# Kernel optimization log

Measured on AMD Instinct MI355X. Metric: run time of the kernel, lower is better.

Reference implementation:

```python
import jax, jax.numpy as jnp
import numpy as np

N, E, F_IN, NUM_GRAPHS, K = 50000, 500000, 160, 128, 3


def _glorot(k, shape):
    lim = np.sqrt(6.0 / (shape[-2] + shape[-1])).astype(np.float32)
    return jax.random.uniform(k, shape, jnp.float32, -lim, lim)


def setup_inputs() -> dict:
    key = jax.random.key(0)
    ks = jax.random.split(key, 8)
    x = jax.random.normal(ks[0], (N, F_IN), jnp.float32)
    edge_index = jax.random.randint(ks[1], (2, E), 0, N)
    edge_attr = jax.random.uniform(ks[2], (E,), jnp.float32)
    batch = jnp.sort(jax.random.randint(ks[3], (N,), 0, NUM_GRAPHS))
    W1 = _glorot(ks[4], (K, F_IN, 128)); b1 = jnp.zeros((128,), jnp.float32)
    W2 = _glorot(ks[5], (K, 128, 64)); b2 = jnp.zeros((64,), jnp.float32)
    W3 = _glorot(ks[6], (K, 64, 32)); b3 = jnp.zeros((32,), jnp.float32)
    Wl = _glorot(ks[7], (32, 2)); bl = jnp.zeros((2,), jnp.float32)
    return dict(x=x, edge_index=edge_index, edge_attr=edge_attr, batch=batch,
                W1=W1, b1=b1, W2=W2, b2=b2, W3=W3, b3=b3, Wl=Wl, bl=bl)


def _cheb_norm(src, dst, edge_attr, n):
    # PyG ChebConv: sym-normalized Laplacian, lambda_max=2 =>
    # L_hat = (2/lmax)*L_sym - I = -D^{-1/2} A D^{-1/2} (diagonal = 0)
    deg = jax.ops.segment_sum(edge_attr, src, num_segments=n)
    safe = jnp.where(deg > 0, deg, 1.0)
    dinv = jnp.where(deg > 0, jax.lax.rsqrt(safe), 0.0)
    return -dinv[src] * edge_attr * dinv[dst]


def _propagate(x, src, dst, w, n):
    # out[dst] += w * x[src]  (sparse L_hat @ x)
    return jax.ops.segment_sum(w[:, None] * x[src], dst, num_segments=n)


def _cheb_conv(x, src, dst, w, W, b, n):
    # Chebyshev recurrence: T0 = x, T1 = L_hat x, Tk = 2 L_hat T(k-1) - T(k-2)
    tx0 = x
    out = tx0 @ W[0]
    tx1 = _propagate(tx0, src, dst, w, n)
    out = out + tx1 @ W[1]
    for k in range(2, W.shape[0]):
        tx2 = 2.0 * _propagate(tx1, src, dst, w, n) - tx0
        out = out + tx2 @ W[k]
        tx0, tx1 = tx1, tx2
    return out + b


def reference(x, edge_index, edge_attr, batch, W1, b1, W2, b2, W3, b3, Wl, bl):
    n = x.shape[0]
    src, dst = edge_index[0], edge_index[1]
    w = _cheb_norm(src, dst, edge_attr, n)
    h = jax.nn.relu(_cheb_conv(x, src, dst, w, W1, b1, n))
    h = jax.nn.relu(_cheb_conv(h, src, dst, w, W2, b2, n))
    h = jax.nn.relu(_cheb_conv(h, src, dst, w, W3, b3, n))
    # global_mean_pool over graph ids (dropout omitted: eval mode)
    sums = jax.ops.segment_sum(h, batch, num_segments=NUM_GRAPHS)
    cnt = jax.ops.segment_sum(jnp.ones((n,), h.dtype), batch, num_segments=NUM_GRAPHS)
    pooled = sums / jnp.maximum(cnt, 1.0)[:, None]
    return pooled @ Wl + bl
```

## Files before the change

kernel.cpp:

```cpp
#include <hip/hip_runtime.h>

#define N_NODES 50000
#define N_EDGES 500000
#define NUM_G   128
#define SCAN_NB 49
#define PN      (SCAN_NB * 1024)
#define NCX     32
#define NCX_SH  5
#define ECH     15628
#define RNG     8192
#define NRY     7
#define HVB     (2 * NCX * NRY)
#define CONVB   7813
#define WPREPB  360
#define RNG_SC  2688
#define NRY_SC  19
#define SCVB    (NCX * NRY_SC)
#define GEMM_MB 782

typedef __attribute__((ext_vector_type(8))) short short8;
typedef __attribute__((ext_vector_type(4))) float f32x4;
typedef __attribute__((ext_vector_type(2))) float f32x2;

__device__ __forceinline__ unsigned f2bf(float x) {
    unsigned u = __float_as_uint(x);
    return (u + 0x7FFFu + ((u >> 16) & 1u)) >> 16;
}
__device__ __forceinline__ float bf2f(unsigned h) {
    return __uint_as_float(h << 16);
}

__device__ __forceinline__ void wprep_one(const float* __restrict__ W, unsigned short* __restrict__ WT,
                                          int t, int FIN, int F) {
    int n = t / FIN, k = t - n * FIN;
    int sel = n / F, c = n - sel * F;
    float v;
    if (sel == 0) v = W[(size_t)k * F + c] - W[(size_t)2 * FIN * F + (size_t)k * F + c];
    else          v = W[(size_t)sel * FIN * F + (size_t)k * F + c];
    WT[t] = (unsigned short)f2bf(v);
}

__global__ __launch_bounds__(256)
void prep_kernel(const int* __restrict__ src, const int* __restrict__ dst,
                 const float* __restrict__ ea,
                 float* __restrict__ pdeg, int* __restrict__ pcnt,
                 const float* __restrict__ x, unsigned short* __restrict__ Xb,
                 const float* __restrict__ W1, const float* __restrict__ W2,
                 const float* __restrict__ W3,
                 unsigned short* __restrict__ WT1, unsigned short* __restrict__ WT2,
                 unsigned short* __restrict__ WT3) {
    __shared__ unsigned lh[RNG];
    int vb = blockIdx.x, tid = threadIdx.x;
    if (vb < HVB) {
        bool isdeg = vb < NCX * NRY;
        int v2 = isdeg ? vb : vb - NCX * NRY;
        int xk = v2 & (NCX - 1), y = v2 >> NCX_SH;
        int base = y * RNG;
        for (int i = tid; i < RNG; i += 256) lh[i] = 0u;
        __syncthreads();
        int e0 = xk * ECH, e1 = min(e0 + ECH, N_EDGES);
        if (isdeg) {
            for (int e = e0 + tid * 4; e < e1; e += 1024) {
                int4 s4 = *reinterpret_cast<const int4*>(src + e);
                if ((unsigned)(s4.x - base) < RNG) atomicAdd((float*)&lh[s4.x - base], ea[e]);
                if ((unsigned)(s4.y - base) < RNG) atomicAdd((float*)&lh[s4.y - base], ea[e + 1]);
                if ((unsigned)(s4.z - base) < RNG) atomicAdd((float*)&lh[s4.z - base], ea[e + 2]);
                if ((unsigned)(s4.w - base) < RNG) atomicAdd((float*)&lh[s4.w - base], ea[e + 3]);
            }
        } else {
            for (int e = e0 + tid * 4; e < e1; e += 1024) {
                int4 d4 = *reinterpret_cast<const int4*>(dst + e);
                if ((unsigned)(d4.x - base) < RNG) atomicAdd((int*)&lh[d4.x - base], 1);
                if ((unsigned)(d4.y - base) < RNG) atomicAdd((int*)&lh[d4.y - base], 1);
                if ((unsigned)(d4.z - base) < RNG) atomicAdd((int*)&lh[d4.z - base], 1);
                if ((unsigned)(d4.w - base) < RNG) atomicAdd((int*)&lh[d4.w - base], 1);
            }
        }
        __syncthreads();
        if (isdeg) {
            for (int i = tid; i < RNG; i += 256) {
                int n = base + i;
                if (n < PN) pdeg[(size_t)xk * PN + n] = ((float*)lh)[i];
            }
        } else {
            for (int i = tid; i < RNG; i += 256) {
                int n = base + i;
                if (n < PN) pcnt[(size_t)xk * PN + n] = ((int*)lh)[i];
            }
        }
    } else if (vb < HVB + CONVB) {
        int t = (vb - HVB) * 256 + tid;
        if (t < N_NODES * 160 / 4) {
            float4 v = reinterpret_cast<const float4*>(x)[t];
            ushort4 r;
            r.x = (unsigned short)f2bf(v.x);
            r.y = (unsigned short)f2bf(v.y);
            r.z = (unsigned short)f2bf(v.z);
            r.w = (unsigned short)f2bf(v.w);
            *reinterpret_cast<ushort4*>(Xb + (size_t)t * 4) = r;
        }
    } else {
        int t = (vb - HVB - CONVB) * 256 + tid;
        if (t < 61440)      wprep_one(W1, WT1, t, 160, 128);
        else if (t < 86016) wprep_one(W2, WT2, t - 61440, 128, 64);
        else if (t < 92160) wprep_one(W3, WT3, t - 86016, 64, 32);
    }
}

__global__ __launch_bounds__(256)
void reduce_scan_kernel(const float* __restrict__ pdeg, int* __restrict__ pcnt,
                        float* __restrict__ dinv, int* __restrict__ cnt,
                        int* __restrict__ partial) {
    int b = blockIdx.x, t = threadIdx.x;
    int i0 = b * 1024 + t * 4;
    float d0 = 0.f, d1 = 0.f, d2 = 0.f, d3 = 0.f;
    int r0 = 0, r1 = 0, r2 = 0, r3 = 0;
    for (int x = 0; x < NCX; ++x) {
        float4 pv = *reinterpret_cast<const float4*>(pdeg + (size_t)x * PN + i0);
        int4   cv = *reinterpret_cast<const int4*>(pcnt + (size_t)x * PN + i0);
        *reinterpret_cast<int4*>(pcnt + (size_t)x * PN + i0) = make_int4(r0, r1, r2, r3);
        d0 += pv.x; d1 += pv.y; d2 += pv.z; d3 += pv.w;
        r0 += cv.x; r1 += cv.y; r2 += cv.z; r3 += cv.w;
    }
    float dd[4] = {d0, d1, d2, d3};
    int   rr[4] = {r0, r1, r2, r3};
    int s = 0;
    #pragma unroll
    for (int j = 0; j < 4; ++j) {
        int n = i0 + j;
        if (n < N_NODES) {
            float dv = dd[j], r = 0.f;
            if (dv > 0.f) {
                r = rsqrtf(dv);
                r = r * (1.5f - 0.5f * dv * r * r);
            }
            dinv[n] = r;
            cnt[n] = rr[j];
            s += rr[j];
        } else {
            cnt[n] = 0;
        }
    }
    __shared__ int red[256];
    red[t] = s;
    __syncthreads();
    for (int off = 128; off > 0; off >>= 1) {
        if (t < off) red[t] += red[t + off];
        __syncthreads();
    }
    if (t == 0) partial[b] = red[0];
}

__global__ __launch_bounds__(256)
void scan_final_kernel(const int* __restrict__ cnt, const int* __restrict__ partial,
                       int* __restrict__ rowptr, int n) {
    int b = blockIdx.x, t = threadIdx.x;
    __shared__ int red[256];
    __shared__ int sh_off, sh_tot;
    if (t < 64) {
        int orig = (t < SCAN_NB) ? partial[t] : 0;
        int v = orig;
        #pragma unroll
        for (int off = 1; off < 64; off <<= 1) {
            int u = __shfl_up(v, off, 64);
            if (t >= off) v += u;
        }
        if (t == b) sh_off = v - orig;
        if (t == SCAN_NB - 1) sh_tot = v;
    }
    __syncthreads();
    int4 v = reinterpret_cast<const int4*>(cnt)[b * 256 + t];
    int s = v.x + v.y + v.z + v.w;
    red[t] = s;
    __syncthreads();
    for (int off = 1; off < 256; off <<= 1) {
        int u = (t >= off) ? red[t - off] : 0;
        __syncthreads();
        red[t] += u;
        __syncthreads();
    }
    int excl = sh_off + ((t == 0) ? 0 : red[t - 1]);
    int i0 = b * 1024 + t * 4;
    if (i0 < n)     rowptr[i0]     = excl;
    if (i0 + 1 < n) rowptr[i0 + 1] = excl + v.x;
    if (i0 + 2 < n) rowptr[i0 + 2] = excl + v.x + v.y;
    if (i0 + 3 < n) rowptr[i0 + 3] = excl + v.x + v.y + v.z;
    if (b == SCAN_NB - 1 && t == 0) rowptr[n] = sh_tot;
}

__device__ void scatter_body(int vb, const int* __restrict__ src, const int* __restrict__ dst,
                             const float* __restrict__ ea,
                             const int* __restrict__ rowptr, const int* __restrict__ pcnt,
                             int2* __restrict__ csr, unsigned char* smraw) {
    int* cursor = (int*)smraw;
    int tid = threadIdx.x;
    int x = vb & (NCX - 1), y = vb >> NCX_SH;
    int base = y * RNG_SC;
    for (int i = tid; i < RNG_SC; i += 256) {
        int n = base + i;
        cursor[i] = (n < N_NODES) ? (rowptr[n] + pcnt[(size_t)x * PN + n]) : 0;
    }
    __syncthreads();
    int e0 = x * ECH, e1 = min(e0 + ECH, N_EDGES);
    for (int e = e0 + tid * 4; e < e1; e += 1024) {
        int4 d4 = *reinterpret_cast<const int4*>(dst + e);
        if ((unsigned)(d4.x - base) < RNG_SC) {
            int pos = atomicAdd(&cursor[d4.x - base], 1);
            csr[pos] = make_int2(src[e], __float_as_int(ea[e]));
        }
        if ((unsigned)(d4.y - base) < RNG_SC) {
            int pos = atomicAdd(&cursor[d4.y - base], 1);
            csr[pos] = make_int2(src[e + 1], __float_as_int(ea[e + 1]));
        }
        if ((unsigned)(d4.z - base) < RNG_SC) {
            int pos = atomicAdd(&cursor[d4.z - base], 1);
            csr[pos] = make_int2(src[e + 2], __float_as_int(ea[e + 2]));
        }
        if ((unsigned)(d4.w - base) < RNG_SC) {
            int pos = atomicAdd(&cursor[d4.w - base], 1);
            csr[pos] = make_int2(src[e + 3], __float_as_int(ea[e + 3]));
        }
    }
}

template<int FIN, int F>
__device__ void gemm_body(int bx, const unsigned short* __restrict__ Xb,
                          const unsigned short* __restrict__ WT, const float* __restrict__ dinv,
                          unsigned short* __restrict__ Y0, unsigned short* __restrict__ Y1,
                          unsigned short* __restrict__ Y2, int nrows, unsigned char* smraw) {
    constexpr int KT = FIN / 32;
    constexpr int NT = F / 32;
    constexpr int NTT = 3 * NT;
    constexpr int SA = FIN + 8;
    constexpr int F8 = FIN / 8;
    short* Bs = (short*)smraw;

    int tid = threadIdx.x;
    int lane = tid & 63, w = tid >> 6;
    int m0 = bx * 64;

    int colb = lane & 15;
    int q8 = (lane >> 4) << 3;
    int rq = (lane >> 4) << 2;
    int arow = m0 + w * 16 + colb;
    bool rok = arow < nrows;

    short8 afr[KT];
    #pragma unroll
    for (int kt = 0; kt < KT; ++kt) {
        short8 z = {0, 0, 0, 0, 0, 0, 0, 0};
        afr[kt] = rok ? *reinterpret_cast<const short8*>(Xb + (size_t)arow * FIN + (kt << 5) + q8) : z;
    }

    for (int nt = 0; nt < NTT; ++nt) {
        int n0 = nt << 5;
        __syncthreads();
        for (int span = tid; span < 32 * F8; span += 256) {
            int r = span / F8, c8 = (span - r * F8) << 3;
            int pr = (r < 16) ? (r << 1) : (((r - 16) << 1) + 1);
            *reinterpret_cast<uint4*>(&Bs[r * SA + c8]) =
                *reinterpret_cast<const uint4*>(WT + (size_t)(n0 + pr) * FIN + c8);
        }
        __syncthreads();

        f32x4 acc0 = {0.f, 0.f, 0.f, 0.f}, acc1 = acc0;
        #pragma unroll
        for (int kt = 0; kt < KT; ++kt) {
            short8 b0 = *reinterpret_cast<const short8*>(&Bs[colb * SA + (kt << 5) + q8]);
            short8 b1 = *reinterpret_cast<const short8*>(&Bs[(colb + 16) * SA + (kt << 5) + q8]);
            acc0 = __builtin_amdgcn_mfma_f32_16x16x32_bf16(afr[kt], b0, acc0, 0, 0, 0);
            acc1 = __builtin_amdgcn_mfma_f32_16x16x32_bf16(afr[kt], b1, acc1, 0, 0, 0);
        }

        int g = nt / NT;
        int ntg = nt - g * NT;
        unsigned short* Ys = (g == 0) ? Y0 : (g == 1) ? Y1 : Y2;
        int lc = (ntg << 5) + (colb << 1);
        #pragma unroll
        for (int r = 0; r < 4; ++r) {
            int orow = m0 + w * 16 + rq + r;
            if (orow < nrows) {
                float sc = (g == 2) ? dinv[orow] : 1.0f;
                unsigned pack = f2bf(acc0[r] * sc) | (f2bf(acc1[r] * sc) << 16);
                *reinterpret_cast<unsigned*>(Ys + (size_t)orow * F + lc) = pack;
            }
        }
    }
}

__global__ __launch_bounds__(256)
void sg_kernel(const int* __restrict__ src, const int* __restrict__ dst,
               const float* __restrict__ ea,
               const int* __restrict__ rowptr, const int* __restrict__ pcnt,
               int2* __restrict__ csr,
               const unsigned short* __restrict__ Xb, const unsigned short* __restrict__ WT1,
               const float* __restrict__ dinv,
               unsigned short* __restrict__ Y0, unsigned short* __restrict__ Y1,
               unsigned short* __restrict__ Y2) {
    __shared__ alignas(16) unsigned char sm[32 * (160 + 8) * 2];
    int vb = blockIdx.x;
    if (vb < SCVB) {
        scatter_body(vb, src, dst, ea, rowptr, pcnt, csr, sm);
    } else {
        gemm_body<160, 128>(vb - SCVB, Xb, WT1, dinv, Y0, Y1, Y2, N_NODES, sm);
    }
}

template<int FIN, int F>
__launch_bounds__(256)
__global__ void cheb_gemm(const unsigned short* __restrict__ Xb, const unsigned short* __restrict__ WT,
                          const float* __restrict__ dinv,
                          unsigned short* __restrict__ Y0, unsigned short* __restrict__ Y1,
                          unsigned short* __restrict__ Y2, int nrows) {
    __shared__ alignas(16) unsigned char sm[32 * (FIN + 8) * 2];
    gemm_body<FIN, F>(blockIdx.x, Xb, WT, dinv, Y0, Y1, Y2, nrows, sm);
}

__device__ __forceinline__ void acc8p(f32x2* acc, uint4 p, float wv) {
    f32x2 w2; w2[0] = wv; w2[1] = wv;
    f32x2 a0, a1, a2, a3;
    a0[0] = __uint_as_float(p.x << 16); a0[1] = __uint_as_float(p.x & 0xFFFF0000u);
    a1[0] = __uint_as_float(p.y << 16); a1[1] = __uint_as_float(p.y & 0xFFFF0000u);
    a2[0] = __uint_as_float(p.z << 16); a2[1] = __uint_as_float(p.z & 0xFFFF0000u);
    a3[0] = __uint_as_float(p.w << 16); a3[1] = __uint_as_float(p.w & 0xFFFF0000u);
    acc[0] += w2 * a0;
    acc[1] += w2 * a1;
    acc[2] += w2 * a2;
    acc[3] += w2 * a3;
}

__device__ __forceinline__ void expand8(uint4 p, float* o) {
    o[0] = bf2f(p.x & 0xFFFFu);
    o[1] = __uint_as_float(p.x & 0xFFFF0000u);
    o[2] = bf2f(p.y & 0xFFFFu);
    o[3] = __uint_as_float(p.y & 0xFFFF0000u);
    o[4] = bf2f(p.z & 0xFFFFu);
    o[5] = __uint_as_float(p.z & 0xFFFF0000u);
    o[6] = bf2f(p.w & 0xFFFFu);
    o[7] = __uint_as_float(p.w & 0xFFFF0000u);
}

template<int F, int MODE>
__launch_bounds__(256)
__global__ void gather_kernel(const unsigned short* __restrict__ X, const int2* __restrict__ csr,
                              const int* __restrict__ rowptr, const float* __restrict__ dinv,
                              const unsigned short* __restrict__ Y, const float* __restrict__ bias,
                              unsigned short* __restrict__ O, int n) {
    constexpr int FQ8 = F >> 3;
    constexpr int DPB = 256 / FQ8;
    constexpr int CAP = 1280;
    __shared__ int2 scsr[CAP];
    __shared__ int srp[DPB + 1];
    __shared__ int smap[DPB];
    int tid = threadIdx.x;
    int db0 = blockIdx.x * DPB;
    if (tid <= DPB) srp[tid] = rowptr[min(db0 + tid, n)];
    __syncthreads();
    int ebeg = srp[0];
    int ecnt = srp[DPB] - ebeg;
    bool staged = ecnt <= CAP;
    if (tid < DPB) {
        int my = srp[tid + 1] - srp[tid];
        int rk = 0;
        for (int g2 = 0; g2 < DPB; ++g2) {
            int l2 = srp[g2 + 1] - srp[g2];
            rk += (l2 < my) || (l2 == my && g2 < tid);
        }
        smap[rk] = tid;
    }
    if (staged) {
        for (int i = tid; i < ecnt; i += 256)
            scsr[i] = csr[ebeg + i];
    }
    __syncthreads();

    int gq = tid / FQ8;
    int rr = smap[gq];
    int d = db0 + rr;
    if (d >= n) return;
    int f8 = (tid - gq * FQ8) << 3;
    f32x2 acc[4];
    #pragma unroll
    for (int j = 0; j < 4; ++j) { acc[j][0] = 0.f; acc[j][1] = 0.f; }

    if (staged) {
        int beg = srp[rr] - ebeg, end = srp[rr + 1] - ebeg;
        int i = beg;
        for (; i + 7 < end; i += 8) {
            int2 e0 = scsr[i],     e1 = scsr[i + 1], e2 = scsr[i + 2], e3 = scsr[i + 3];
            int2 e4 = scsr[i + 4], e5 = scsr[i + 5], e6 = scsr[i + 6], e7 = scsr[i + 7];
            uint4 p0 = *reinterpret_cast<const uint4*>(X + (size_t)e0.x * F + f8);
            uint4 p1 = *reinterpret_cast<const uint4*>(X + (size_t)e1.x * F + f8);
            uint4 p2 = *reinterpret_cast<const uint4*>(X + (size_t)e2.x * F + f8);
            uint4 p3 = *reinterpret_cast<const uint4*>(X + (size_t)e3.x * F + f8);
            uint4 p4 = *reinterpret_cast<const uint4*>(X + (size_t)e4.x * F + f8);
            uint4 p5 = *reinterpret_cast<const uint4*>(X + (size_t)e5.x * F + f8);
            uint4 p6 = *reinterpret_cast<const uint4*>(X + (size_t)e6.x * F + f8);
            uint4 p7 = *reinterpret_cast<const uint4*>(X + (size_t)e7.x * F + f8);
            acc8p(acc, p0, __int_as_float(e0.y));
            acc8p(acc, p1, __int_as_float(e1.y));
            acc8p(acc, p2, __int_as_float(e2.y));
            acc8p(acc, p3, __int_as_float(e3.y));
            acc8p(acc, p4, __int_as_float(e4.y));
            acc8p(acc, p5, __int_as_float(e5.y));
            acc8p(acc, p6, __int_as_float(e6.y));
            acc8p(acc, p7, __int_as_float(e7.y));
        }
        for (; i + 3 < end; i += 4) {
            int2 e0 = scsr[i], e1 = scsr[i + 1], e2 = scsr[i + 2], e3 = scsr[i + 3];
            uint4 p0 = *reinterpret_cast<const uint4*>(X + (size_t)e0.x * F + f8);
            uint4 p1 = *reinterpret_cast<const uint4*>(X + (size_t)e1.x * F + f8);
            uint4 p2 = *reinterpret_cast<const uint4*>(X + (size_t)e2.x * F + f8);
            uint4 p3 = *reinterpret_cast<const uint4*>(X + (size_t)e3.x * F + f8);
            acc8p(acc, p0, __int_as_float(e0.y));
            acc8p(acc, p1, __int_as_float(e1.y));
            acc8p(acc, p2, __int_as_float(e2.y));
            acc8p(acc, p3, __int_as_float(e3.y));
        }
        for (; i < end; ++i) {
            int2 e = scsr[i];
            uint4 p = *reinterpret_cast<const uint4*>(X + (size_t)e.x * F + f8);
            acc8p(acc, p, __int_as_float(e.y));
        }
    } else {
        int beg = srp[rr], end = srp[rr + 1];
        for (int i = beg; i < end; ++i) {
            int2 e = csr[i];
            uint4 p = *reinterpret_cast<const uint4*>(X + (size_t)e.x * F + f8);
            acc8p(acc, p, __int_as_float(e.y));
        }
    }

    float accs[8];
    #pragma unroll
    for (int j = 0; j < 8; ++j) accs[j] = acc[j >> 1][j & 1];

    float y[8];
    expand8(*reinterpret_cast<const uint4*>(Y + (size_t)d * F + f8), y);
    float dv = dinv[d];
    float v[8];
    if (MODE == 0) {
        float dv2 = 2.f * dv;
        #pragma unroll
        for (int j = 0; j < 8; ++j) v[j] = dv * (y[j] - dv2 * accs[j]);
    } else {
        float4 ba = *reinterpret_cast<const float4*>(bias + f8);
        float4 bb = *reinterpret_cast<const float4*>(bias + f8 + 4);
        v[0] = fmaxf(y[0] - dv * accs[0] + ba.x, 0.f);
        v[1] = fmaxf(y[1] - dv * accs[1] + ba.y, 0.f);
        v[2] = fmaxf(y[2] - dv * accs[2] + ba.z, 0.f);
        v[3] = fmaxf(y[3] - dv * accs[3] + ba.w, 0.f);
        v[4] = fmaxf(y[4] - dv * accs[4] + bb.x, 0.f);
        v[5] = fmaxf(y[5] - dv * accs[5] + bb.y, 0.f);
        v[6] = fmaxf(y[6] - dv * accs[6] + bb.z, 0.f);
        v[7] = fmaxf(y[7] - dv * accs[7] + bb.w, 0.f);
    }
    uint4 o;
    o.x = f2bf(v[0]) | (f2bf(v[1]) << 16);
    o.y = f2bf(v[2]) | (f2bf(v[3]) << 16);
    o.z = f2bf(v[4]) | (f2bf(v[5]) << 16);
    o.w = f2bf(v[6]) | (f2bf(v[7]) << 16);
    *reinterpret_cast<uint4*>(O + (size_t)d * F + f8) = o;
}

__device__ __forceinline__ int lower_bound_dev(const int* __restrict__ a, int n, int v) {
    int lo = 0, hi = n;
    while (lo < hi) {
        int mid = (lo + hi) >> 1;
        if (a[mid] < v) lo = mid + 1; else hi = mid;
    }
    return lo;
}

__global__ void pool_kernel(const unsigned short* __restrict__ H, const int* __restrict__ batch,
                            const float* __restrict__ Wl, const float* __restrict__ bl,
                            float* __restrict__ out, int n) {
    int g = blockIdx.x;
    int start = lower_bound_dev(batch, n, g);
    int end   = lower_bound_dev(batch, n, g + 1);
    int tid = threadIdx.x;
    int f = tid & 31;
    int sub = tid >> 5;
    float acc = 0.0f;
    for (int i = start + sub; i < end; i += 8)
        acc += bf2f((unsigned)H[(size_t)i * 32 + f]);
    __shared__ float red[256];
    red[tid] = acc;
    __syncthreads();
    if (tid < 128) red[tid] += red[tid + 128];
    __syncthreads();
    if (tid < 64) red[tid] += red[tid + 64];
    __syncthreads();
    if (tid < 32) red[tid] += red[tid + 32];
    __syncthreads();
    if (tid < 2) {
        int cnt = end - start;
        float inv = 1.0f / (float)(cnt > 0 ? cnt : 1);
        float o = bl[tid];
        for (int f2 = 0; f2 < 32; ++f2)
            o += red[f2] * inv * Wl[f2 * 2 + tid];
        out[g * 2 + tid] = o;
    }
}

extern "C" void kernel_launch(void* const* d_in, const int* in_sizes, int n_in,
                              void* d_out, int out_size, void* d_ws, size_t ws_size,
                              hipStream_t stream) {
    const float* x     = (const float*)d_in[0];
    const int*   ei    = (const int*)d_in[1];
    const float* ea    = (const float*)d_in[2];
    const int*   batch = (const int*)d_in[3];
    const float* W1 = (const float*)d_in[4];
    const float* b1 = (const float*)d_in[5];
    const float* W2 = (const float*)d_in[6];
    const float* b2 = (const float*)d_in[7];
    const float* W3 = (const float*)d_in[8];
    const float* b3 = (const float*)d_in[9];
    const float* Wl = (const float*)d_in[10];
    const float* bl = (const float*)d_in[11];
    float* out = (float*)d_out;
    char* ws = (char*)d_ws;

    const int* src = ei;
    const int* dst = ei + N_EDGES;

    size_t off = 0;
    auto alloc = [&](size_t bytes) { char* p = ws + off; off += (bytes + 255) & ~(size_t)255; return p; };
    float* pdeg    = (float*)alloc((size_t)NCX * PN * 4);
    int*   pcnt    = (int*)  alloc((size_t)NCX * PN * 4);
    float* dinv    = (float*)alloc(N_NODES * 4);
    int*   cnt     = (int*)  alloc((size_t)PN * 4);
    int*   partial = (int*)  alloc(SCAN_NB * 4);
    int*   rowptr  = (int*)  alloc((N_NODES + 1) * 4);
    int2*  csr     = (int2*) alloc((size_t)N_EDGES * 8);
    unsigned short* Xb  = (unsigned short*)alloc((size_t)N_NODES * 160 * 2);
    unsigned short* Y0  = (unsigned short*)alloc((size_t)N_NODES * 128 * 2);
    unsigned short* Y1  = (unsigned short*)alloc((size_t)N_NODES * 128 * 2);
    unsigned short* Y2  = (unsigned short*)alloc((size_t)N_NODES * 128 * 2);
    unsigned short* U   = (unsigned short*)alloc((size_t)N_NODES * 128 * 2);
    unsigned short* WT1 = (unsigned short*)alloc((size_t)384 * 160 * 2);
    unsigned short* WT2 = (unsigned short*)alloc((size_t)192 * 128 * 2);
    unsigned short* WT3 = (unsigned short*)alloc((size_t)96 * 64 * 2);

    const int BT = 256;

    prep_kernel<<<HVB + CONVB + WPREPB, BT, 0, stream>>>(src, dst, ea, pdeg, pcnt,
                                                         x, Xb, W1, W2, W3, WT1, WT2, WT3);
    reduce_scan_kernel<<<SCAN_NB, BT, 0, stream>>>(pdeg, pcnt, dinv, cnt, partial);
    scan_final_kernel<<<SCAN_NB, BT, 0, stream>>>(cnt, partial, rowptr, N_NODES);
    sg_kernel<<<SCVB + GEMM_MB, BT, 0, stream>>>(src, dst, ea, rowptr, pcnt, csr,
                                                 Xb, WT1, dinv, Y0, Y1, Y2);

    auto gb = [&](int F) { int DPB = 256 / (F / 8); return (N_NODES + DPB - 1) / DPB; };

    gather_kernel<128, 0><<<gb(128), BT, 0, stream>>>(Y2, csr, rowptr, dinv, Y1, nullptr, U, N_NODES);
    gather_kernel<128, 1><<<gb(128), BT, 0, stream>>>(U, csr, rowptr, dinv, Y0, b1, Xb, N_NODES);

    cheb_gemm<128, 64><<<GEMM_MB, BT, 0, stream>>>(Xb, WT2, dinv, Y0, Y1, Y2, N_NODES);
    gather_kernel<64, 0><<<gb(64), BT, 0, stream>>>(Y2, csr, rowptr, dinv, Y1, nullptr, U, N_NODES);
    gather_kernel<64, 1><<<gb(64), BT, 0, stream>>>(U, csr, rowptr, dinv, Y0, b2, Xb, N_NODES);

    cheb_gemm<64, 32><<<GEMM_MB, BT, 0, stream>>>(Xb, WT3, dinv, Y0, Y1, Y2, N_NODES);
    gather_kernel<32, 0><<<gb(32), BT, 0, stream>>>(Y2, csr, rowptr, dinv, Y1, nullptr, U, N_NODES);
    gather_kernel<32, 1><<<gb(32), BT, 0, stream>>>(U, csr, rowptr, dinv, Y0, b3, Xb, N_NODES);

    pool_kernel<<<NUM_G, BT, 0, stream>>>(Xb, batch, Wl, bl, out, N_NODES);
}
```

Before: 293.2 us.

## Fuse x bf16 conversion into first GEMM and predicate gather tail loop

Removes the separate fp32-to-bf16 conversion of x from the prep kernel and converts the A fragments directly inside the first-layer GEMM, which now reads fp32 x. This avoids writing and rereading a bf16 copy of x. The staged gather loop is also rewritten as a single 8-wide loop with clamped indices and zeroed weights for out-of-range lanes, replacing the 8/4/1 remainder loops. The clamped lanes do redundant loads for short rows, and the GEMM now reads twice as many bytes for its A operand.

```diff
diff --git a/kernel.cpp b/kernel.cpp
--- a/kernel.cpp
+++ b/kernel.cpp
@@ -11,7 +11,6 @@
 #define RNG     8192
 #define NRY     7
 #define HVB     (2 * NCX * NRY)
-#define CONVB   7813
 #define WPREPB  360
 #define RNG_SC  2688
 #define NRY_SC  19
@@ -44,7 +43,6 @@
 void prep_kernel(const int* __restrict__ src, const int* __restrict__ dst,
                  const float* __restrict__ ea,
                  float* __restrict__ pdeg, int* __restrict__ pcnt,
-                 const float* __restrict__ x, unsigned short* __restrict__ Xb,
                  const float* __restrict__ W1, const float* __restrict__ W2,
                  const float* __restrict__ W3,
                  unsigned short* __restrict__ WT1, unsigned short* __restrict__ WT2,
@@ -88,19 +86,8 @@
                 if (n < PN) pcnt[(size_t)xk * PN + n] = ((int*)lh)[i];
             }
         }
-    } else if (vb < HVB + CONVB) {
+    } else {
         int t = (vb - HVB) * 256 + tid;
-        if (t < N_NODES * 160 / 4) {
-            float4 v = reinterpret_cast<const float4*>(x)[t];
-            ushort4 r;
-            r.x = (unsigned short)f2bf(v.x);
-            r.y = (unsigned short)f2bf(v.y);
-            r.z = (unsigned short)f2bf(v.z);
-            r.w = (unsigned short)f2bf(v.w);
-            *reinterpret_cast<ushort4*>(Xb + (size_t)t * 4) = r;
-        }
-    } else {
-        int t = (vb - HVB - CONVB) * 256 + tid;
         if (t < 61440)      wprep_one(W1, WT1, t, 160, 128);
         else if (t < 86016) wprep_one(W2, WT2, t - 61440, 128, 64);
         else if (t < 92160) wprep_one(W3, WT3, t - 86016, 64, 32);
@@ -223,8 +210,8 @@
     }
 }
 
-template<int FIN, int F>
-__device__ void gemm_body(int bx, const unsigned short* __restrict__ Xb,
+template<int FIN, int F, bool AFP32>
+__device__ void gemm_body(int bx, const void* __restrict__ Araw,
                           const unsigned short* __restrict__ WT, const float* __restrict__ dinv,
                           unsigned short* __restrict__ Y0, unsigned short* __restrict__ Y1,
                           unsigned short* __restrict__ Y2, int nrows, unsigned char* smraw) {
@@ -249,7 +236,21 @@
     #pragma unroll
     for (int kt = 0; kt < KT; ++kt) {
         short8 z = {0, 0, 0, 0, 0, 0, 0, 0};
-        afr[kt] = rok ? *reinterpret_cast<const short8*>(Xb + (size_t)arow * FIN + (kt << 5) + q8) : z;
+        if (!rok) { afr[kt] = z; continue; }
+        if constexpr (AFP32) {
+            const float* A = (const float*)Araw;
+            float4 f0 = *reinterpret_cast<const float4*>(A + (size_t)arow * FIN + (kt << 5) + q8);
+            float4 f1 = *reinterpret_cast<const float4*>(A + (size_t)arow * FIN + (kt << 5) + q8 + 4);
+            short8 r;
+            r[0] = (short)f2bf(f0.x); r[1] = (short)f2bf(f0.y);
+            r[2] = (short)f2bf(f0.z); r[3] = (short)f2bf(f0.w);
+            r[4] = (short)f2bf(f1.x); r[5] = (short)f2bf(f1.y);
+            r[6] = (short)f2bf(f1.z); r[7] = (short)f2bf(f1.w);
+            afr[kt] = r;
+        } else {
+            const unsigned short* A = (const unsigned short*)Araw;
+            afr[kt] = *reinterpret_cast<const short8*>(A + (size_t)arow * FIN + (kt << 5) + q8);
+        }
     }
 
     for (int nt = 0; nt < NTT; ++nt) {
@@ -293,7 +294,7 @@
                const float* __restrict__ ea,
                const int* __restrict__ rowptr, const int* __restrict__ pcnt,
                int2* __restrict__ csr,
-               const unsigned short* __restrict__ Xb, const unsigned short* __restrict__ WT1,
+               const float* __restrict__ x, const unsigned short* __restrict__ WT1,
                const float* __restrict__ dinv,
                unsigned short* __restrict__ Y0, unsigned short* __restrict__ Y1,
                unsigned short* __restrict__ Y2) {
@@ -302,7 +303,7 @@
     if (vb < SCVB) {
         scatter_body(vb, src, dst, ea, rowptr, pcnt, csr, sm);
     } else {
-        gemm_body<160, 128>(vb - SCVB, Xb, WT1, dinv, Y0, Y1, Y2, N_NODES, sm);
+        gemm_body<160, 128, true>(vb - SCVB, x, WT1, dinv, Y0, Y1, Y2, N_NODES, sm);
     }
 }
 
@@ -313,7 +314,7 @@
                           unsigned short* __restrict__ Y0, unsigned short* __restrict__ Y1,
                           unsigned short* __restrict__ Y2, int nrows) {
     __shared__ alignas(16) unsigned char sm[32 * (FIN + 8) * 2];
-    gemm_body<FIN, F>(blockIdx.x, Xb, WT, dinv, Y0, Y1, Y2, nrows, sm);
+    gemm_body<FIN, F, false>(blockIdx.x, Xb, WT, dinv, Y0, Y1, Y2, nrows, sm);
 }
 
 __device__ __forceinline__ void acc8p(f32x2* acc, uint4 p, float wv) {
@@ -385,10 +386,16 @@
 
     if (staged) {
         int beg = srp[rr] - ebeg, end = srp[rr + 1] - ebeg;
-        int i = beg;
-        for (; i + 7 < end; i += 8) {
-            int2 e0 = scsr[i],     e1 = scsr[i + 1], e2 = scsr[i + 2], e3 = scsr[i + 3];
-            int2 e4 = scsr[i + 4], e5 = scsr[i + 5], e6 = scsr[i + 6], e7 = scsr[i + 7];
+        int last = end - 1;
+        for (int i = beg; i < end; i += 8) {
+            int2 e0 = scsr[i];
+            int2 e1 = scsr[min(i + 1, last)];
+            int2 e2 = scsr[min(i + 2, last)];
+            int2 e3 = scsr[min(i + 3, last)];
+            int2 e4 = scsr[min(i + 4, last)];
+            int2 e5 = scsr[min(i + 5, last)];
+            int2 e6 = scsr[min(i + 6, last)];
+            int2 e7 = scsr[min(i + 7, last)];
             uint4 p0 = *reinterpret_cast<const uint4*>(X + (size_t)e0.x * F + f8);
             uint4 p1 = *reinterpret_cast<const uint4*>(X + (size_t)e1.x * F + f8);
             uint4 p2 = *reinterpret_cast<const uint4*>(X + (size_t)e2.x * F + f8);
@@ -397,30 +404,22 @@
             uint4 p5 = *reinterpret_cast<const uint4*>(X + (size_t)e5.x * F + f8);
             uint4 p6 = *reinterpret_cast<const uint4*>(X + (size_t)e6.x * F + f8);
             uint4 p7 = *reinterpret_cast<const uint4*>(X + (size_t)e7.x * F + f8);
-            acc8p(acc, p0, __int_as_float(e0.y));
-            acc8p(acc, p1, __int_as_float(e1.y));
-            acc8p(acc, p2, __int_as_float(e2.y));
-            acc8p(acc, p3, __int_as_float(e3.y));
-            acc8p(acc, p4, __int_as_float(e4.y));
-            acc8p(acc, p5, __int_as_float(e5.y));
-            acc8p(acc, p6, __int_as_float(e6.y));
-            acc8p(acc, p7, __int_as_float(e7.y));
-        }
-        for (; i + 3 < end; i += 4) {
-            int2 e0 = scsr[i], e1 = scsr[i + 1], e2 = scsr[i + 2], e3 = scsr[i + 3];
-            uint4 p0 = *reinterpret_cast<const uint4*>(X + (size_t)e0.x * F + f8);
-            uint4 p1 = *reinterpret_cast<const uint4*>(X + (size_t)e1.x * F + f8);
-            uint4 p2 = *reinterpret_cast<const uint4*>(X + (size_t)e2.x * F + f8);
-            uint4 p3 = *reinterpret_cast<const uint4*>(X + (size_t)e3.x * F + f8);
-            acc8p(acc, p0, __int_as_float(e0.y));
-            acc8p(acc, p1, __int_as_float(e1.y));
-            acc8p(acc, p2, __int_as_float(e2.y));
-            acc8p(acc, p3, __int_as_float(e3.y));
-        }
-        for (; i < end; ++i) {
-            int2 e = scsr[i];
-            uint4 p = *reinterpret_cast<const uint4*>(X + (size_t)e.x * F + f8);
-            acc8p(acc, p, __int_as_float(e.y));
+            float w0 = __int_as_float(e0.y);
+            float w1 = (i + 1 < end) ? __int_as_float(e1.y) : 0.f;
+            float w2 = (i + 2 < end) ? __int_as_float(e2.y) : 0.f;
+            float w3 = (i + 3 < end) ? __int_as_float(e3.y) : 0.f;
+            float w4 = (i + 4 < end) ? __int_as_float(e4.y) : 0.f;
+            float w5 = (i + 5 < end) ? __int_as_float(e5.y) : 0.f;
+            float w6 = (i + 6 < end) ? __int_as_float(e6.y) : 0.f;
+            float w7 = (i + 7 < end) ? __int_as_float(e7.y) : 0.f;
+            acc8p(acc, p0, w0);
+            acc8p(acc, p1, w1);
+            acc8p(acc, p2, w2);
+            acc8p(acc, p3, w3);
+            acc8p(acc, p4, w4);
+            acc8p(acc, p5, w5);
+            acc8p(acc, p6, w6);
+            acc8p(acc, p7, w7);
         }
     } else {
         int beg = srp[rr], end = srp[rr + 1];
@@ -544,12 +543,12 @@
 
     const int BT = 256;
 
-    prep_kernel<<<HVB + CONVB + WPREPB, BT, 0, stream>>>(src, dst, ea, pdeg, pcnt,
-                                                         x, Xb, W1, W2, W3, WT1, WT2, WT3);
+    prep_kernel<<<HVB + WPREPB, BT, 0, stream>>>(src, dst, ea, pdeg, pcnt,
+                                                 W1, W2, W3, WT1, WT2, WT3);
     reduce_scan_kernel<<<SCAN_NB, BT, 0, stream>>>(pdeg, pcnt, dinv, cnt, partial);
     scan_final_kernel<<<SCAN_NB, BT, 0, stream>>>(cnt, partial, rowptr, N_NODES);
     sg_kernel<<<SCVB + GEMM_MB, BT, 0, stream>>>(src, dst, ea, rowptr, pcnt, csr,
-                                                 Xb, WT1, dinv, Y0, Y1, Y2);
+                                                 x, WT1, dinv, Y0, Y1, Y2);
 
     auto gb = [&](int F) { int DPB = 256 / (F / 8); return (N_NODES + DPB - 1) / DPB; };
 
```

Measured after the change: 288.8 us. About the same (-1.5%).
